# Performance work log

Measured on AMD Instinct MI355X. Metric: run time of the kernel, lower is better.

Reference implementation:

```python
import jax, jax.numpy as jnp
import numpy as np

NUM_EMBEDDINGS = 1024
EMBEDDING_DIM = 64
COMMITMENT_COST = 0.25


def setup_inputs() -> dict:
    key = jax.random.key(0)
    k1, k2 = jax.random.split(key)
    inputs = jax.random.normal(k1, (64, 2048, EMBEDDING_DIM), dtype=jnp.float32)
    # matches torch init: uniform(-1/K, 1/K)
    codebook = jax.random.uniform(
        k2, (NUM_EMBEDDINGS, EMBEDDING_DIM), dtype=jnp.float32,
        minval=-1.0 / NUM_EMBEDDINGS, maxval=1.0 / NUM_EMBEDDINGS)
    return {"inputs": inputs, "codebook": codebook}


def reference(inputs, codebook):
    orig_shape = inputs.shape
    flat = inputs.reshape(-1, EMBEDDING_DIM)            # [N, D]
    # squared Euclidean distances (same argmin as torch.cdist)
    d2 = (jnp.sum(flat * flat, axis=1, keepdims=True)   # [N, 1]
          - 2.0 * flat @ codebook.T                      # [N, K]
          + jnp.sum(codebook * codebook, axis=1)[None, :])
    encoding_indices = jnp.argmin(d2, axis=1)            # [N] int
    quantized = codebook[encoding_indices].reshape(orig_shape)

    e_latent_loss = jnp.mean((jax.lax.stop_gradient(quantized) - inputs) ** 2)
    q_latent_loss = jnp.mean((quantized - jax.lax.stop_gradient(inputs)) ** 2)
    loss = q_latent_loss + COMMITMENT_COST * e_latent_loss

    # straight-through estimator
    quantized_ste = inputs + jax.lax.stop_gradient(quantized - inputs)
    return quantized_ste, loss, encoding_indices
```

## Files before the change

### kernel.cpp

```cpp
#include <hip/hip_runtime.h>


#define NROWS  131072
#define DIM    64
#define KCB    1024
#define QSIZE  (NROWS * DIM)

typedef unsigned long long u64;
typedef unsigned int u32;
typedef unsigned short ushortx;
typedef __attribute__((ext_vector_type(8))) short short8v;
typedef __attribute__((ext_vector_type(4))) float f32x4;

__device__ __forceinline__ u32 umin32(u32 a, u32 b) { return a < b ? a : b; }
__device__ __forceinline__ u32 umax32(u32 a, u32 b) { return a > b ? a : b; }

__device__ __forceinline__ ushortx f2bf(float f) {
    u32 u = __float_as_uint(f);
    u32 r = u + 0x7FFFu + ((u >> 16) & 1u);
    return (ushortx)(r >> 16);
}
__device__ __forceinline__ float bf2f(ushortx h) {
    return __uint_as_float(((u32)h) << 16);
}

__global__ __launch_bounds__(256) void vq_prep(const float* __restrict__ cb,
                                               float* __restrict__ csq,
                                               float* __restrict__ cs18b,
                                               ushortx* __restrict__ cbsw,
                                               float* __restrict__ loss_slot) {
    const int gid = blockIdx.x * 256 + threadIdx.x;
    const int k  = gid >> 2;
    const int qt = gid & 3;
    const float* c = cb + k * DIM;

    float aq = 0.f;
    #pragma unroll
    for (int d = 0; d < 16; ++d) {
        const float v = c[16 * qt + d];
        aq = fmaf(v, v, aq);
    }
    const float s1 = aq + __shfl_xor(aq, 1, 64);
    const float s2 = s1 + __shfl_xor(s1, 2, 64);
    if (qt == 0) {
        csq[k]   = s2;
        cs18b[k] = s2 * 262144.0f + 131072.0f;
    }

    const int ct = k >> 4;
    const int j  = k & 15;
    #pragma unroll
    for (int cc = 0; cc < 2; ++cc) {
        const int c8 = 2 * qt + cc;
        const int h  = c8 >> 2;
        const int qq = c8 & 3;
        const int L  = qq * 16 + j;
        union { ushortx u[8]; short8v v; } uh, ul;
        #pragma unroll
        for (int e = 0; e < 8; ++e) {
            const float g = c[c8 * 8 + e] * -524288.0f;
            const ushortx hh = f2bf(g);
            uh.u[e] = hh;
            ul.u[e] = f2bf(g - bf2f(hh));
        }
        *reinterpret_cast<short8v*>(cbsw + ct * 2048 + h * 512 + L * 8) = uh.v;
        *reinterpret_cast<short8v*>(cbsw + ct * 2048 + 1024 + h * 512 + L * 8) = ul.v;
    }
    if (gid == 0) *loss_slot = 0.f;
}

__global__ __launch_bounds__(256, 4) void vq_main(const float* __restrict__ x,
                                                  const float* __restrict__ cb,
                                                  const float* __restrict__ csq,
                                                  const float* __restrict__ cs18b,
                                                  const ushortx* __restrict__ cbsw,
                                                  float* __restrict__ out_q,
                                                  float* __restrict__ out_loss,
                                                  float* __restrict__ out_idx) {
    __shared__ u32   sTop[4][32][3];
    __shared__ int   sFinal[128];
    __shared__ float sLoss[4];

    const int tid  = threadIdx.x;
    const int lane = tid & 63;
    const int wid  = tid >> 6;
    const size_t rowbase = (size_t)blockIdx.x * 128;
    const int wrow0 = wid * 32;
    const int lcol  = lane & 15;
    const int lkq   = lane >> 4;

    short8v Ah[2][2], Al[2][2];
    #pragma unroll
    for (int t = 0; t < 2; ++t)
        #pragma unroll
        for (int h = 0; h < 2; ++h) {
            const float* xp = x + (rowbase + (size_t)(wrow0 + t * 16 + lcol)) * DIM
                              + h * 32 + lkq * 8;
            const float4 u0 = *reinterpret_cast<const float4*>(xp);
            const float4 u1 = *reinterpret_cast<const float4*>(xp + 4);
            const float xv[8] = {u0.x, u0.y, u0.z, u0.w, u1.x, u1.y, u1.z, u1.w};
            union { ushortx u[8]; short8v v; } uh, ul;
            #pragma unroll
            for (int j = 0; j < 8; ++j) {
                const ushortx hh = f2bf(xv[j]);
                uh.u[j] = hh;
                ul.u[j] = f2bf(xv[j] - bf2f(hh));
            }
            Ah[t][h] = uh.v;
            Al[t][h] = ul.v;
        }

    u32 k1[8], k2[8], k3[8];
    #pragma unroll
    for (int s = 0; s < 8; ++s) { k1[s] = ~0u; k2[s] = ~0u; k3[s] = ~0u; }

    u32 nlane = (u32)lcol;
    const ushortx* bp = cbsw + (size_t)lane * 8;

    short8v pBh0 = *reinterpret_cast<const short8v*>(bp);
    short8v pBh1 = *reinterpret_cast<const short8v*>(bp + 512);
    short8v pBl0 = *reinterpret_cast<const short8v*>(bp + 1024);
    short8v pBl1 = *reinterpret_cast<const short8v*>(bp + 1536);
    float   pcs  = cs18b[nlane];

    #pragma unroll 1
    for (int ct = 0; ct < 64; ++ct) {
        const short8v Bh0 = pBh0, Bh1 = pBh1, Bl0 = pBl0, Bl1 = pBl1;
        const float csb = pcs;
        bp += 2048;
        pBh0 = *reinterpret_cast<const short8v*>(bp);
        pBh1 = *reinterpret_cast<const short8v*>(bp + 512);
        pBl0 = *reinterpret_cast<const short8v*>(bp + 1024);
        pBl1 = *reinterpret_cast<const short8v*>(bp + 1536);
        pcs  = cs18b[nlane + 16];

        #pragma unroll
        for (int t = 0; t < 2; ++t) {
            f32x4 acc = (f32x4){csb, csb, csb, csb};
            acc = __builtin_amdgcn_mfma_f32_16x16x32_bf16(Ah[t][0], Bh0, acc, 0, 0, 0);
            acc = __builtin_amdgcn_mfma_f32_16x16x32_bf16(Al[t][0], Bh0, acc, 0, 0, 0);
            acc = __builtin_amdgcn_mfma_f32_16x16x32_bf16(Ah[t][0], Bl0, acc, 0, 0, 0);
            acc = __builtin_amdgcn_mfma_f32_16x16x32_bf16(Ah[t][1], Bh1, acc, 0, 0, 0);
            acc = __builtin_amdgcn_mfma_f32_16x16x32_bf16(Al[t][1], Bh1, acc, 0, 0, 0);
            acc = __builtin_amdgcn_mfma_f32_16x16x32_bf16(Ah[t][1], Bl1, acc, 0, 0, 0);
            #pragma unroll
            for (int r = 0; r < 4; ++r) {
                const u32 key = ((u32)acc[r] << 10) | nlane;
                const int s = t * 4 + r;
                const u32 nk1 = umin32(key, k1[s]);
                const u32 mx  = umax32(key, k1[s]);
                const u32 nk2 = umin32(k2[s], mx);
                const u32 mx2 = umax32(k2[s], mx);
                k3[s] = umin32(k3[s], mx2);
                k1[s] = nk1; k2[s] = nk2;
            }
        }
        nlane += 16;
    }

    #pragma unroll
    for (int s = 0; s < 8; ++s) {
        u32 a1 = k1[s], a2 = k2[s], a3 = k3[s];
        #pragma unroll
        for (int mask = 1; mask <= 8; mask <<= 1) {
            const u32 b1 = __shfl_xor(a1, mask, 64);
            const u32 b2 = __shfl_xor(a2, mask, 64);
            const u32 b3 = __shfl_xor(a3, mask, 64);
            const u32 c1 = umin32(a1, b1), d1 = umax32(a1, b1);
            const u32 c2 = umin32(a2, b2);
            const u32 o3 = umin32(umax32(d1, c2), umin32(a3, b3));
            a1 = c1; a2 = umin32(d1, c2); a3 = o3;
        }
        k1[s] = a1; k2[s] = a2; k3[s] = a3;
    }
    if (lcol < 8) {
        const int j = lcol, g = lkq;
        const int row = (j >> 2) * 16 + g * 4 + (j & 3);
        sTop[wid][row][0] = k1[j]; sTop[wid][row][1] = k2[j]; sTop[wid][row][2] = k3[j];
    }
    __syncthreads();

    if (lane < 32) {
        const int row = wrow0 + lane;
        const u32 K1 = sTop[wid][lane][0];
        const u32 K2 = sTop[wid][lane][1];
        const u32 K3 = sTop[wid][lane][2];
        int idx = (int)(K1 & 1023u);
        const u32 m1q = K1 >> 10, m2q = K2 >> 10;
        if (m2q - m1q <= 48u) {
            const float* xr = x + (rowbase + (size_t)row) * DIM;
            float4 xv[16];
            #pragma unroll
            for (int q = 0; q < 16; ++q) xv[q] = reinterpret_cast<const float4*>(xr)[q];
            float p[4];
            #pragma unroll
            for (int q = 0; q < 4; ++q) {
                float a = 0.f;
                #pragma unroll
                for (int e = 0; e < 4; ++e) {
                    const float4 v = xv[4 * q + e];
                    a = fmaf(v.x, v.x, a); a = fmaf(v.y, v.y, a);
                    a = fmaf(v.z, v.z, a); a = fmaf(v.w, v.w, a);
                }
                p[q] = a;
            }
            const float asq = (p[0] + p[1]) + (p[2] + p[3]);
            const u32 Mq = (u32)fmaf(asq, 0.126f, 24.0f);
            u64 best = ~0ull;
            #pragma unroll 1
            for (int c = 0; c < 3; ++c) {
                const u32 Kc = c == 0 ? K1 : (c == 1 ? K2 : K3);
                const u32 mq = Kc >> 10;
                if (c > 0 && (mq - m1q) > Mq) break;
                const int n = (int)(Kc & 1023u);
                const float4* cr = reinterpret_cast<const float4*>(cb + (size_t)n * DIM);
                float acc = 0.f;
                #pragma unroll
                for (int q = 0; q < 16; ++q) {
                    const float4 c4 = cr[q], v = xv[q];
                    acc = fmaf(v.x, c4.x, acc); acc = fmaf(v.y, c4.y, acc);
                    acc = fmaf(v.z, c4.z, acc); acc = fmaf(v.w, c4.w, acc);
                }
                const float tt = asq - 2.0f * acc;
                const float dd = tt + csq[n];
                const u64 kk = ((u64)__float_as_uint(dd) << 32) | (u32)n;
                best = kk < best ? kk : best;
            }
            idx = (int)(u32)best;
        }
        sFinal[row] = idx;
        out_idx[rowbase + row] = (float)idx;
    }
    __syncthreads();

    #pragma unroll 1
    for (int sub = 0; sub < 2; ++sub) {
        const size_t base = (rowbase + 64 * sub) * DIM;
        float lsum = 0.f;
        #pragma unroll 4
        for (int i = tid; i < 64 * DIM; i += 256) {
            const int r = i >> 6;
            const int d = i & 63;
            const int kb = sFinal[64 * sub + r];
            const float q  = cb[(size_t)kb * DIM + d];
            const float xe = x[base + i];
            out_q[base + i] = xe + (q - xe);
            const float df = q - xe;
            lsum = fmaf(df, df, lsum);
        }
        #pragma unroll
        for (int off = 32; off; off >>= 1) lsum += __shfl_down(lsum, off, 64);
        if (lane == 0) sLoss[wid] = lsum;
        __syncthreads();
        if (tid == 0) {
            const float tot = (sLoss[0] + sLoss[1]) + (sLoss[2] + sLoss[3]);
            atomicAdd(out_loss, tot * (1.25f / 8388608.0f));
        }
        __syncthreads();
    }
}

extern "C" void kernel_launch(void* const* d_in, const int* in_sizes, int n_in,
                              void* d_out, int out_size, void* d_ws, size_t ws_size,
                              hipStream_t stream) {
    const float* x  = (const float*)d_in[0];
    const float* cb = (const float*)d_in[1];
    float* out      = (float*)d_out;
    float* out_loss = out + QSIZE;
    float* out_idx  = out + QSIZE + 1;

    float*   csq   = (float*)d_ws;
    float*   cs18b = csq + 1024;
    ushortx* cbsw  = (ushortx*)(csq + 2048);

    vq_prep<<<16, 256, 0, stream>>>(cb, csq, cs18b, cbsw, out_loss);
    vq_main<<<NROWS / 128, 256, 0, stream>>>(x, cb, csq, cs18b, cbsw,
                                             out, out_loss, out_idx);
}
```

Before: 161.6 us.

## Apply distance scale after MFMA, drop B prefetch, tighten exact-rescore thresholds

```diff
diff --git a/kernel.cpp b/kernel.cpp
--- a/kernel.cpp
+++ b/kernel.cpp
@@ -58,10 +58,10 @@
         union { ushortx u[8]; short8v v; } uh, ul;
         #pragma unroll
         for (int e = 0; e < 8; ++e) {
-            const float g = c[c8 * 8 + e] * -524288.0f;
-            const ushortx hh = f2bf(g);
+            const float f = c[c8 * 8 + e];
+            const ushortx hh = f2bf(f);
             uh.u[e] = hh;
-            ul.u[e] = f2bf(g - bf2f(hh));
+            ul.u[e] = f2bf(f - bf2f(hh));
         }
         *reinterpret_cast<short8v*>(cbsw + ct * 2048 + h * 512 + L * 8) = uh.v;
         *reinterpret_cast<short8v*>(cbsw + ct * 2048 + 1024 + h * 512 + L * 8) = ul.v;
@@ -117,26 +117,16 @@
     u32 nlane = (u32)lcol;
     const ushortx* bp = cbsw + (size_t)lane * 8;
 
-    short8v pBh0 = *reinterpret_cast<const short8v*>(bp);
-    short8v pBh1 = *reinterpret_cast<const short8v*>(bp + 512);
-    short8v pBl0 = *reinterpret_cast<const short8v*>(bp + 1024);
-    short8v pBl1 = *reinterpret_cast<const short8v*>(bp + 1536);
-    float   pcs  = cs18b[nlane];
-
     #pragma unroll 1
     for (int ct = 0; ct < 64; ++ct) {
-        const short8v Bh0 = pBh0, Bh1 = pBh1, Bl0 = pBl0, Bl1 = pBl1;
-        const float csb = pcs;
-        bp += 2048;
-        pBh0 = *reinterpret_cast<const short8v*>(bp);
-        pBh1 = *reinterpret_cast<const short8v*>(bp + 512);
-        pBl0 = *reinterpret_cast<const short8v*>(bp + 1024);
-        pBl1 = *reinterpret_cast<const short8v*>(bp + 1536);
-        pcs  = cs18b[nlane + 16];
-
+        const short8v Bh0 = *reinterpret_cast<const short8v*>(bp);
+        const short8v Bh1 = *reinterpret_cast<const short8v*>(bp + 512);
+        const short8v Bl0 = *reinterpret_cast<const short8v*>(bp + 1024);
+        const short8v Bl1 = *reinterpret_cast<const short8v*>(bp + 1536);
+        const float csb = cs18b[nlane];
         #pragma unroll
         for (int t = 0; t < 2; ++t) {
-            f32x4 acc = (f32x4){csb, csb, csb, csb};
+            f32x4 acc = (f32x4){0.f, 0.f, 0.f, 0.f};
             acc = __builtin_amdgcn_mfma_f32_16x16x32_bf16(Ah[t][0], Bh0, acc, 0, 0, 0);
             acc = __builtin_amdgcn_mfma_f32_16x16x32_bf16(Al[t][0], Bh0, acc, 0, 0, 0);
             acc = __builtin_amdgcn_mfma_f32_16x16x32_bf16(Ah[t][0], Bl0, acc, 0, 0, 0);
@@ -145,7 +135,8 @@
             acc = __builtin_amdgcn_mfma_f32_16x16x32_bf16(Ah[t][1], Bl1, acc, 0, 0, 0);
             #pragma unroll
             for (int r = 0; r < 4; ++r) {
-                const u32 key = ((u32)acc[r] << 10) | nlane;
+                const float m18 = fmaf(acc[r], -524288.0f, csb);
+                const u32 key = ((u32)m18 << 10) | nlane;
                 const int s = t * 4 + r;
                 const u32 nk1 = umin32(key, k1[s]);
                 const u32 mx  = umax32(key, k1[s]);
@@ -155,7 +146,7 @@
                 k1[s] = nk1; k2[s] = nk2;
             }
         }
-        nlane += 16;
+        bp += 2048; nlane += 16;
     }
 
     #pragma unroll
@@ -187,7 +178,7 @@
         const u32 K3 = sTop[wid][lane][2];
         int idx = (int)(K1 & 1023u);
         const u32 m1q = K1 >> 10, m2q = K2 >> 10;
-        if (m2q - m1q <= 48u) {
+        if (m2q - m1q <= 26u) {
             const float* xr = x + (rowbase + (size_t)row) * DIM;
             float4 xv[16];
             #pragma unroll
@@ -205,7 +196,7 @@
                 p[q] = a;
             }
             const float asq = (p[0] + p[1]) + (p[2] + p[3]);
-            const u32 Mq = (u32)fmaf(asq, 0.126f, 24.0f);
+            const u32 Mq = (u32)fmaf(asq, 0.126f, 5.0f);
             u64 best = ~0ull;
             #pragma unroll 1
             for (int c = 0; c < 3; ++c) {
```

After: 155.9 us. 3.6% less time.
